# Kernel optimization log

Measured on AMD Instinct MI355X. Metric: run time of the kernel, lower is better.

The kernel has to match this reference:

```python
import jax, jax.numpy as jnp
import numpy as np

N, D, H, C, E, M = 8192, 256, 256, 64, 262144, 2048
WD = 5e-4   # weight_decay
HP1 = 0.9
TAU = 0.5


def _l2norm(x, eps=1e-12):
    n = jnp.sqrt(jnp.sum(x * x, axis=1, keepdims=True))
    return x / jnp.maximum(n, eps)


def setup_inputs() -> dict:
    key = jax.random.key(0)
    ks = jax.random.split(key, 20)
    s = 0.05
    return dict(
        features=jax.random.uniform(ks[0], (N, D), dtype=jnp.float32),
        support=jax.random.uniform(ks[1], (N, N), dtype=jnp.float32) / N,  # mimics normalized adjacency scale
        labels=jax.random.uniform(ks[2], (N, C), dtype=jnp.float32),
        mat01_intra=jax.random.uniform(ks[3], (M, M), dtype=jnp.float32),
        mat01_inter=jax.random.uniform(ks[4], (M, M), dtype=jnp.float32),
        W0=jax.random.normal(ks[5], (D, H), dtype=jnp.float32) * s,
        b0=jnp.zeros((H,), jnp.float32),
        W1=jax.random.normal(ks[6], (H, C), dtype=jnp.float32) * s,
        b1=jnp.zeros((C,), jnp.float32),
        Wh0=jax.random.normal(ks[7], (D, H), dtype=jnp.float32) * s,
        bh0=jnp.zeros((H,), jnp.float32),
        Wh1=jax.random.normal(ks[8], (H, C), dtype=jnp.float32) * s,
        bh1=jnp.zeros((C,), jnp.float32),
        Wc=jax.random.normal(ks[9], (2 * C, 1), dtype=jnp.float32) * s,
        bc=jnp.zeros((1,), jnp.float32),
        edge_pos_i=jax.random.randint(ks[10], (E,), 0, N, dtype=jnp.int32),
        edge_pos_j=jax.random.randint(ks[11], (E,), 0, N, dtype=jnp.int32),
        train_idx=jax.random.randint(ks[12], (M,), 0, N, dtype=jnp.int32),
        mask=jax.random.randint(ks[13], (N,), 0, 2, dtype=jnp.int32),
    )


def _forward(features, support, labels, mat01_intra, mat01_inter,
             W0, b0, W1, b1, Wh0, bh0, Wh1, bh1, Wc, bc,
             edge_pos_i, edge_pos_j, train_idx, mask):
    # --- GCN branch: relu(S (X W0) + b0) -> S (h0 W1) + b1
    h0 = jax.nn.relu(support @ (features @ W0) + b0)
    h1 = support @ (h0 @ W1) + b1
    gcn_n = _l2norm(h1)
    # --- HGCN branch (2-layer GCN stand-in)
    g0 = jax.nn.relu(support @ (features @ Wh0) + bh0)
    hgcn = support @ (g0 @ Wh1) + bh1
    hgcn_n = _l2norm(hgcn)
    outputs = _l2norm(0.6 * gcn_n + 0.4 * hgcn_n)

    # masked softmax cross entropy
    maskf = mask.astype(jnp.float32)
    maskf = maskf / jnp.mean(maskf)
    logp = jax.nn.log_softmax(outputs, axis=1)
    loss_ce = jnp.mean(-jnp.sum(labels * logp, axis=1) * maskf)

    # edge gathers + contra MLP: log sigmoid of linear on concatenated pairs
    yi_g, yj_g = gcn_n[edge_pos_i], gcn_n[edge_pos_j]
    yi_h, yj_h = hgcn_n[edge_pos_i], hgcn_n[edge_pos_j]
    z1 = jnp.concatenate([yi_g, yj_h], axis=1) @ Wc + bc  # [E,1]
    z2 = jnp.concatenate([yi_h, yj_g], axis=1) @ Wc + bc
    p_e_xy = -jnp.mean(jax.nn.log_sigmoid(z1)) - jnp.mean(jax.nn.log_sigmoid(z2))

    # unsupervised contrastive over full NxN
    cd1 = jnp.exp((gcn_n @ hgcn_n.T) / TAU)      # [N,N]
    pn1 = jnp.diagonal(cd1) / jnp.mean(cd1, axis=1)
    cd2 = jnp.exp((hgcn_n @ gcn_n.T) / TAU)
    pn2 = jnp.diagonal(cd2) / jnp.mean(cd2, axis=1)
    contra = -HP1 * jnp.mean(jnp.log(jnp.concatenate([pn1, pn2], axis=0)))

    # supervised contrastive on train subset
    rowsum = jnp.sum(mat01_intra, axis=1)  # mat01_intra_rowsum buffer
    h1t, h2t = gcn_n[train_idx], hgcn_n[train_idx]
    Mn = train_idx.shape[0]

    def sup(a, b):
        hc = jnp.exp((a @ b.T) / TAU)            # [M,M]
        sp = jnp.sum(hc * mat01_intra, axis=1)
        sn = (jnp.sum(hc * mat01_inter, axis=1) + sp) / (Mn - 1)
        return (sp / rowsum) / sn

    pns = jnp.concatenate([sup(h1t, h2t), sup(h2t, h1t)], axis=0)
    contra = contra + (-HP1 * jnp.mean(jnp.log(pns)))

    wd = WD * 0.5 * (jnp.sum(W0 ** 2) + jnp.sum(b0 ** 2) + jnp.sum(W1 ** 2)
                     + jnp.sum(b1 ** 2) + jnp.sum(Wc ** 2) + jnp.sum(bc ** 2))
    loss = loss_ce + 0.4 * p_e_xy + contra + wd  # HGCN.loss = 0 for the stand-in

    correct = (jnp.argmax(outputs, axis=1) == jnp.argmax(labels, axis=1)).astype(jnp.float32)
    accuracy = jnp.mean(correct * maskf)
    return outputs, loss, accuracy


def reference(features, support, labels, mat01_intra, mat01_inter,
              W0, b0, W1, b1, Wh0, bh0, Wh1, bh1, Wc, bc,
              edge_pos_i, edge_pos_j, train_idx, mask):
    return _forward(features, support, labels, mat01_intra, mat01_inter,
                    W0, b0, W1, b1, Wh0, bh0, Wh1, bh1, Wc, bc,
                    edge_pos_i, edge_pos_j, train_idx, mask)
```

## Files before the change

kernel.cpp:

```cpp
#include <hip/hip_runtime.h>

#define DEVI __device__ __forceinline__

typedef __bf16 bf16x8 __attribute__((ext_vector_type(8)));
typedef float f32x4 __attribute__((ext_vector_type(4)));
typedef unsigned short u16;
typedef unsigned long long ull;

constexpr int NN = 8192;
constexpr int EE = 262144;

constexpr size_t OF_WT0b = 0;
constexpr size_t OF_WT1b = OF_WT0b + 65536;
constexpr size_t OF_BIA0 = OF_WT1b + 32768;
constexpr size_t OF_X16  = OF_BIA0 + 512;
constexpr size_t OF_A    = OF_X16 + 1048576;
constexpr size_t OF_D    = OF_A + 2097152;
constexpr size_t OF_VEC  = OF_D + 524288;
constexpr size_t OF_SD   = OF_VEC;
constexpr size_t OF_R1   = OF_SD + 8192;
constexpr size_t OF_R2   = OF_R1 + 16384;
constexpr size_t OF_AG   = OF_R2 + 16384;
constexpr size_t OF_BG   = OF_AG + 8192;
constexpr size_t OF_AH   = OF_BG + 8192;
constexpr size_t OF_BH   = OF_AH + 8192;
constexpr size_t OF_SP1  = OF_BH + 8192;
constexpr size_t OF_SNR1 = OF_SP1 + 2048;
constexpr size_t OF_SP2  = OF_SNR1 + 2048;
constexpr size_t OF_SNR2 = OF_SP2 + 2048;
constexpr size_t OF_RSI  = OF_SNR2 + 2048;
constexpr size_t OF_SCAL = OF_RSI + 2048;
constexpr size_t WS_SMALL = OF_SCAL + 16;
constexpr size_t OF_S16  = WS_SMALL;
constexpr size_t OF_E    = OF_S16 + 33554432;
constexpr size_t WS_NEED = OF_E + 8388608;

#define SC_CE 0
#define SC_MASK 1
#define SC_ACC 2
#define SC_E1 3
#define SC_E2 4
#define SC_C1 5
#define SC_C2 6
#define SC_WD 7

DEVI u16 bf1(float f) { __bf16 h = (__bf16)f; return __builtin_bit_cast(u16, h); }
DEVI unsigned int bf2(float a, float b) {
  return (unsigned)bf1(a) | ((unsigned)bf1(b) << 16);
}
DEVI ull bf4(float4 v) {
  return (ull)bf2(v.x, v.y) | ((ull)bf2(v.z, v.w) << 32);
}
DEVI float b2f(u16 h) { return __uint_as_float(((unsigned)h) << 16); }
DEVI float lo16(unsigned w) { return __uint_as_float(w << 16); }
DEVI float hi16(unsigned w) { return __uint_as_float(w & 0xffff0000u); }
DEVI f32x4 mfma16(bf16x8 a, bf16x8 b, f32x4 c) {
  return __builtin_amdgcn_mfma_f32_16x16x32_bf16(a, b, c, 0, 0, 0);
}
DEVI float wsum64(float v) {
  #pragma unroll
  for (int m = 1; m < 64; m <<= 1) v += __shfl_xor(v, m, 64);
  return v;
}
DEVI float wmax64(float v) {
  #pragma unroll
  for (int m = 1; m < 64; m <<= 1) v = fmaxf(v, __shfl_xor(v, m, 64));
  return v;
}
DEVI int wargmax64(float v, int idx) {
  #pragma unroll
  for (int m = 1; m < 64; m <<= 1) {
    float ov = __shfl_xor(v, m, 64);
    int   oi = __shfl_xor(idx, m, 64);
    if (ov > v || (ov == v && oi < idx)) { v = ov; idx = oi; }
  }
  return idx;
}
DEVI void blockAtomicAdd(float* dst, float v) {
  __shared__ float red[4];
  const int tid = threadIdx.x;
  v = wsum64(v);
  __syncthreads();
  if ((tid & 63) == 0) red[tid >> 6] = v;
  __syncthreads();
  if (tid == 0) atomicAdd(dst, red[0] + red[1] + red[2] + red[3]);
}
DEVI float logsig(float z) {
  return fminf(z, 0.f) - log1pf(__expf(-fabsf(z)));
}

__global__ __launch_bounds__(256)
void cvtbf(const float* __restrict__ src, u16* __restrict__ dst, long n8) {
  long stride = (long)gridDim.x * 256;
  for (long i = (long)blockIdx.x * 256 + threadIdx.x; i < n8; i += stride) {
    long off = i << 3;
    float4 a = *(const float4*)(src + off);
    float4 b = *(const float4*)(src + off + 4);
    uint4 o;
    o.x = bf2(a.x, a.y); o.y = bf2(a.z, a.w);
    o.z = bf2(b.x, b.y); o.w = bf2(b.z, b.w);
    *(uint4*)(dst + off) = o;
  }
}

__global__ void prep(const float* __restrict__ W0, const float* __restrict__ Wh0,
                     const float* __restrict__ W1, const float* __restrict__ Wh1,
                     const float* __restrict__ b0, const float* __restrict__ bh0,
                     u16* __restrict__ wt0, u16* __restrict__ wt1,
                     float* __restrict__ bias0) {
  int t = blockIdx.x * 256 + threadIdx.x;
  if (t < 131072) {
    int j = t >> 8, k = t & 255;
    wt0[t] = bf1((j < 256) ? W0[k * 256 + j] : Wh0[k * 256 + (j - 256)]);
  } else if (t < 196608) {
    int u = t - 131072;
    int j = u >> 9, k = u & 511;
    float v = 0.f;
    if (j < 64)  { if (k < 256)  v = W1 [k * 64 + j]; }
    else         { if (k >= 256) v = Wh1[(k - 256) * 64 + (j - 64)]; }
    wt1[u] = bf1(v);
  } else if (t < 197120) {
    int j = t - 196608;
    bias0[j] = (j < 256) ? b0[j] : bh0[j - 256];
  }
}

template <int FM, int FN, int SWZ, int MLOC, int NLOG, int MINB>
__global__ __launch_bounds__(256, MINB)
void gemm_a(const u16* __restrict__ A16, const u16* __restrict__ B16,
            u16* __restrict__ Cv, int K, int Ntot, int ksteps, size_t splitStride) {
  constexpr int BM = 32 * FM, BN = 32 * FN;
  constexpr int NSEG = (BM + BN) / 16;
  constexpr int SPW = NSEG / 4;
  __shared__ __align__(16) u16 As[2][BM * 32];
  __shared__ __align__(16) u16 Bs[2][BN * 32];
  const int tid = threadIdx.x;
  const int l = tid & 63, wid = tid >> 6;
  const int wr = wid >> 1, wc = wid & 1;
  const int fr = l & 15, fg = l >> 4;

  int m0, n0;
  if (SWZ) {
    int id = blockIdx.x + gridDim.x * blockIdx.y;
    int e = id & 7, s = id >> 3;
    m0 = (e * MLOC + (s >> NLOG)) * BM;
    n0 = (s & ((1 << NLOG) - 1)) * BN;
  } else {
    m0 = blockIdx.y * BM;
    n0 = blockIdx.x * BN;
  }
  const size_t kbase = (size_t)blockIdx.z * ksteps * 32;

  const u16* gsrc[SPW];
  u16* ld0[SPW];
  u16* ld1[SPW];
  #pragma unroll
  for (int q = 0; q < SPW; ++q) {
    int s = q * 4 + wid;
    if (s < BM / 16) {
      gsrc[q] = A16 + (size_t)(m0 + s * 16 + (l & 15)) * K + kbase + ((l >> 4) << 3);
      ld0[q] = &As[0][s << 9];
      ld1[q] = &As[1][s << 9];
    } else {
      int t2 = s - BM / 16;
      gsrc[q] = B16 + (size_t)(n0 + t2 * 16 + (l & 15)) * K + kbase + ((l >> 4) << 3);
      ld0[q] = &Bs[0][t2 << 9];
      ld1[q] = &Bs[1][t2 << 9];
    }
  }
  auto stageTo = [&](int buf, int ks2) {
    int koff = ks2 * 32;
    #pragma unroll
    for (int q = 0; q < SPW; ++q) {
      u16* d = buf ? ld1[q] : ld0[q];
      __builtin_amdgcn_global_load_lds(
          (const __attribute__((address_space(1))) void*)(gsrc[q] + koff),
          (__attribute__((address_space(3))) void*)d, 16, 0, 0);
    }
  };

  f32x4 zero = {0.f, 0.f, 0.f, 0.f};
  f32x4 acc[FM][FN];
  #pragma unroll
  for (int i = 0; i < FM; ++i)
    #pragma unroll
    for (int j = 0; j < FN; ++j) acc[i][j] = zero;

  stageTo(0, 0);
  int cur = 0;
  for (int ks = 0; ks < ksteps; ++ks) {
    __syncthreads();
    if (ks + 1 < ksteps) stageTo(cur ^ 1, ks + 1);
    bf16x8 af[FM], bfv[FN];
    #pragma unroll
    for (int i = 0; i < FM; ++i)
      af[i] = *(const bf16x8*)&As[cur][((wr * FM + i) << 9) + (l << 3)];
    #pragma unroll
    for (int j = 0; j < FN; ++j)
      bfv[j] = *(const bf16x8*)&Bs[cur][((wc * FN + j) << 9) + (l << 3)];
    #pragma unroll
    for (int i = 0; i < FM; ++i)
      #pragma unroll
      for (int j = 0; j < FN; ++j)
        acc[i][j] = mfma16(af[i], bfv[j], acc[i][j]);
    cur ^= 1;
  }

  u16* outp = Cv + (size_t)blockIdx.z * splitStride;
  #pragma unroll
  for (int i = 0; i < FM; ++i)
    #pragma unroll
    for (int j = 0; j < FN; ++j)
      #pragma unroll
      for (int r = 0; r < 4; ++r) {
        int grow = m0 + wr * 16 * FM + i * 16 + (fg << 2) + r;
        int gcol = n0 + wc * 16 * FN + j * 16 + fr;
        outp[(size_t)grow * Ntot + gcol] = bf1(acc[i][j][r]);
      }
}

template <int NS>
__global__ __launch_bounds__(256)
void relupack(const u16* __restrict__ z, const float* __restrict__ bias,
              u16* __restrict__ h16) {
  int t = blockIdx.x * 256 + threadIdx.x;
  int off = t << 3;
  int col = off & 511;
  float4 c0 = *(const float4*)(bias + col);
  float4 c1 = *(const float4*)(bias + col + 4);
  float r[8] = {c0.x, c0.y, c0.z, c0.w, c1.x, c1.y, c1.z, c1.w};
  #pragma unroll
  for (int s = 0; s < NS; ++s) {
    uint4 a = *(const uint4*)(z + (size_t)s * 8192 * 512 + off);
    r[0] += lo16(a.x); r[1] += hi16(a.x);
    r[2] += lo16(a.y); r[3] += hi16(a.y);
    r[4] += lo16(a.z); r[5] += hi16(a.z);
    r[6] += lo16(a.w); r[7] += hi16(a.w);
  }
  uint4 o;
  o.x = bf2(fmaxf(r[0], 0.f), fmaxf(r[1], 0.f));
  o.y = bf2(fmaxf(r[2], 0.f), fmaxf(r[3], 0.f));
  o.z = bf2(fmaxf(r[4], 0.f), fmaxf(r[5], 0.f));
  o.w = bf2(fmaxf(r[6], 0.f), fmaxf(r[7], 0.f));
  *(uint4*)(h16 + off) = o;
}

template <int NS>
__global__ __launch_bounds__(256)
void rowstats(const u16* __restrict__ Z2p, const float* __restrict__ b1,
              const float* __restrict__ bh1, const float* __restrict__ labels,
              const int* __restrict__ mask, const float* __restrict__ Wc,
              float* __restrict__ outp, u16* __restrict__ gcn16, u16* __restrict__ hgcn16,
              float* __restrict__ sd, float* __restrict__ ag, float* __restrict__ bg,
              float* __restrict__ ah, float* __restrict__ bh, float* __restrict__ scal) {
  const int tid = threadIdx.x, l = tid & 63, w = tid >> 6;
  const float wa = Wc[l], wb = Wc[64 + l];
  const float bb1 = b1[l], bbh1 = bh1[l];
  float s_ce = 0.f, s_mk = 0.f, s_ac = 0.f;
  for (int it = 0; it < 8; ++it) {
    int row = blockIdx.x * 32 + it * 4 + w;
    float h1 = bb1, hg = bbh1;
    #pragma unroll
    for (int s = 0; s < NS; ++s) {
      h1 += b2f(Z2p[(size_t)s * 1048576 + row * 128 + l]);
      hg += b2f(Z2p[(size_t)s * 1048576 + row * 128 + 64 + l]);
    }
    float n1 = wsum64(h1 * h1);
    float gn = h1 / fmaxf(sqrtf(n1), 1e-12f);
    float n2 = wsum64(hg * hg);
    float hn = hg / fmaxf(sqrtf(n2), 1e-12f);
    float oc = 0.6f * gn + 0.4f * hn;
    float n3 = wsum64(oc * oc);
    float o = oc / fmaxf(sqrtf(n3), 1e-12f);
    size_t ro = (size_t)row * 64 + l;
    outp[ro] = o; gcn16[ro] = bf1(gn); hgcn16[ro] = bf1(hn);
    float sdv = wsum64(gn * hn);
    float vag = wsum64(gn * wa), vbg = wsum64(gn * wb);
    float vah = wsum64(hn * wa), vbh = wsum64(hn * wb);
    float lab = labels[ro];
    float mx = wmax64(o);
    float se = wsum64(__expf(o - mx));
    float lse = mx + __logf(se);
    float slab = wsum64(lab);
    float slo = wsum64(lab * o);
    int am_o = wargmax64(o, l);
    int am_l = wargmax64(lab, l);
    if (l == 0) {
      sd[row] = sdv; ag[row] = vag; bg[row] = vbg; ah[row] = vah; bh[row] = vbh;
      float mk = (float)mask[row];
      s_ce += (lse * slab - slo) * mk;
      s_mk += mk;
      s_ac += (am_o == am_l) ? mk : 0.f;
    }
  }
  blockAtomicAdd(&scal[SC_CE], s_ce);
  blockAtomicAdd(&scal[SC_MASK], s_mk);
  blockAtomicAdd(&scal[SC_ACC], s_ac);
}

__global__ __launch_bounds__(256)
void rowsumexp2(const u16* __restrict__ G16, const u16* __restrict__ H16,
                float* __restrict__ R1, float* __restrict__ R2) {
  constexpr int PK = 72;
  __shared__ __align__(16) u16 At[64 * PK];
  __shared__ __align__(16) u16 Bt[64 * PK];
  const int bx = blockIdx.x;
  const int nh = bx >> 8, r = bx & 255, dir = r >> 7;
  const u16* __restrict__ A = dir ? H16 : G16;
  const u16* __restrict__ B = dir ? G16 : H16;
  float* __restrict__ out = (dir ? R2 : R1) + nh * 8192;
  const int tid = threadIdx.x, l = tid & 63, w = tid >> 6;
  const int m0 = (r & 127) * 64;
  #pragma unroll
  for (int p = 0; p < 2; ++p) {
    int idx = p * 256 + tid, row = idx >> 3, kq = (idx & 7) << 3;
    *(uint4*)&At[row * PK + kq] = *(const uint4*)(A + (size_t)(m0 + row) * 64 + kq);
  }
  __syncthreads();
  const int fr = l & 15, fg = l >> 4;
  bf16x8 a0 = *(const bf16x8*)&At[(w * 16 + fr) * PK + (fg << 3)];
  bf16x8 a1 = *(const bf16x8*)&At[(w * 16 + fr) * PK + 32 + (fg << 3)];
  float rs0 = 0.f, rs1 = 0.f, rs2 = 0.f, rs3 = 0.f;
  const int nbeg = nh * 4096;
  for (int n0 = nbeg; n0 < nbeg + 4096; n0 += 64) {
    __syncthreads();
    #pragma unroll
    for (int p = 0; p < 2; ++p) {
      int idx = p * 256 + tid, row = idx >> 3, kq = (idx & 7) << 3;
      *(uint4*)&Bt[row * PK + kq] = *(const uint4*)(B + (size_t)(n0 + row) * 64 + kq);
    }
    __syncthreads();
    #pragma unroll
    for (int jn = 0; jn < 4; ++jn) {
      bf16x8 b0 = *(const bf16x8*)&Bt[(jn * 16 + fr) * PK + (fg << 3)];
      bf16x8 b1 = *(const bf16x8*)&Bt[(jn * 16 + fr) * PK + 32 + (fg << 3)];
      f32x4 c = {0.f, 0.f, 0.f, 0.f};
      c = mfma16(a0, b0, c);
      c = mfma16(a1, b1, c);
      rs0 += __expf(c[0] * 2.0f);
      rs1 += __expf(c[1] * 2.0f);
      rs2 += __expf(c[2] * 2.0f);
      rs3 += __expf(c[3] * 2.0f);
    }
  }
  #pragma unroll
  for (int m = 1; m < 16; m <<= 1) {
    rs0 += __shfl_xor(rs0, m, 64);
    rs1 += __shfl_xor(rs1, m, 64);
    rs2 += __shfl_xor(rs2, m, 64);
    rs3 += __shfl_xor(rs3, m, 64);
  }
  if (fr == 0) {
    int rb = m0 + w * 16 + fg * 4;
    out[rb + 0] = rs0; out[rb + 1] = rs1; out[rb + 2] = rs2; out[rb + 3] = rs3;
  }
}

__global__ __launch_bounds__(256)
void supstats2(const u16* __restrict__ G16, const u16* __restrict__ H16,
               const int* __restrict__ tidx,
               const float* __restrict__ Wi_g, const float* __restrict__ We_g,
               float* __restrict__ SP1, float* __restrict__ SNR1,
               float* __restrict__ SP2, float* __restrict__ SNR2) {
  constexpr int PK = 72;
  __shared__ __align__(16) u16 At[64 * PK];
  __shared__ __align__(16) u16 Bt[64 * PK];
  __shared__ float Ws0[64 * 68];
  __shared__ float Ws1[64 * 68];
  const int bx = blockIdx.x;
  const int chunk = bx >> 6, sub = bx & 63, dir = sub >> 5;
  const u16* __restrict__ A = dir ? H16 : G16;
  const u16* __restrict__ B = dir ? G16 : H16;
  float* __restrict__ sp_out  = dir ? SP2 : SP1;
  float* __restrict__ sn_out  = dir ? SNR2 : SNR1;
  const int tid = threadIdx.x, l = tid & 63, w = tid >> 6;
  const int m0 = (sub & 31) * 64;
  #pragma unroll
  for (int p = 0; p < 2; ++p) {
    int idx = p * 256 + tid, row = idx >> 3, kq = (idx & 7) << 3;
    int gr = tidx[m0 + row];
    *(uint4*)&At[row * PK + kq] = *(const uint4*)(A + (size_t)gr * 64 + kq);
  }
  __syncthreads();
  const int fr = l & 15, fg = l >> 4;
  bf16x8 a0 = *(const bf16x8*)&At[(w * 16 + fr) * PK + (fg << 3)];
  bf16x8 a1 = *(const bf16x8*)&At[(w * 16 + fr) * PK + 32 + (fg << 3)];
  float sp0 = 0, sp1 = 0, sp2 = 0, sp3 = 0, sn0 = 0, sn1 = 0, sn2 = 0, sn3 = 0;
  const int nbeg = chunk * 512;
  for (int n0 = nbeg; n0 < nbeg + 512; n0 += 64) {
    __syncthreads();
    #pragma unroll
    for (int p = 0; p < 2; ++p) {
      int idx = p * 256 + tid, row = idx >> 3, kq = (idx & 7) << 3;
      int gr = tidx[n0 + row];
      *(uint4*)&Bt[row * PK + kq] = *(const uint4*)(B + (size_t)gr * 64 + kq);
    }
    #pragma unroll
    for (int p = 0; p < 4; ++p) {
      int idx = p * 256 + tid, row = idx >> 4, kq = (idx & 15) << 2;
      *(float4*)&Ws0[row * 68 + kq] = *(const float4*)(Wi_g + (size_t)(m0 + row) * 2048 + n0 + kq);
      *(float4*)&Ws1[row * 68 + kq] = *(const float4*)(We_g + (size_t)(m0 + row) * 2048 + n0 + kq);
    }
    __syncthreads();
    #pragma unroll
    for (int jn = 0; jn < 4; ++jn) {
      bf16x8 b0 = *(const bf16x8*)&Bt[(jn * 16 + fr) * PK + (fg << 3)];
      bf16x8 b1 = *(const bf16x8*)&Bt[(jn * 16 + fr) * PK + 32 + (fg << 3)];
      f32x4 c = {0.f, 0.f, 0.f, 0.f};
      c = mfma16(a0, b0, c);
      c = mfma16(a1, b1, c);
      int cl = jn * 16 + fr;
      int rl = w * 16 + fg * 4;
      float e0 = __expf(c[0] * 2.0f);
      float e1 = __expf(c[1] * 2.0f);
      float e2 = __expf(c[2] * 2.0f);
      float e3 = __expf(c[3] * 2.0f);
      sp0 += e0 * Ws0[(rl + 0) * 68 + cl]; sn0 += e0 * Ws1[(rl + 0) * 68 + cl];
      sp1 += e1 * Ws0[(rl + 1) * 68 + cl]; sn1 += e1 * Ws1[(rl + 1) * 68 + cl];
      sp2 += e2 * Ws0[(rl + 2) * 68 + cl]; sn2 += e2 * Ws1[(rl + 2) * 68 + cl];
      sp3 += e3 * Ws0[(rl + 3) * 68 + cl]; sn3 += e3 * Ws1[(rl + 3) * 68 + cl];
    }
  }
  #pragma unroll
  for (int m = 1; m < 16; m <<= 1) {
    sp0 += __shfl_xor(sp0, m, 64); sn0 += __shfl_xor(sn0, m, 64);
    sp1 += __shfl_xor(sp1, m, 64); sn1 += __shfl_xor(sn1, m, 64);
    sp2 += __shfl_xor(sp2, m, 64); sn2 += __shfl_xor(sn2, m, 64);
    sp3 += __shfl_xor(sp3, m, 64); sn3 += __shfl_xor(sn3, m, 64);
  }
  if (fr == 0) {
    int rb = m0 + w * 16 + fg * 4;
    atomicAdd(&sp_out[rb + 0], sp0); atomicAdd(&sn_out[rb + 0], sn0);
    atomicAdd(&sp_out[rb + 1], sp1); atomicAdd(&sn_out[rb + 1], sn1);
    atomicAdd(&sp_out[rb + 2], sp2); atomicAdd(&sn_out[rb + 2], sn2);
    atomicAdd(&sp_out[rb + 3], sp3); atomicAdd(&sn_out[rb + 3], sn3);
  }
}

__global__ __launch_bounds__(256)
void rowsum2048(const float* __restrict__ Wi, float* __restrict__ rsi) {
  int l = threadIdx.x & 63, w = threadIdx.x >> 6;
  int row = blockIdx.x * 4 + w;
  float s = 0.f;
  #pragma unroll
  for (int p = 0; p < 8; ++p) {
    int c = (p * 64 + l) << 2;
    float4 v = *(const float4*)(Wi + (size_t)row * 2048 + c);
    s += v.x + v.y + v.z + v.w;
  }
  s = wsum64(s);
  if (l == 0) rsi[row] = s;
}

__global__ __launch_bounds__(256)
void edgered(const int* __restrict__ ei, const int* __restrict__ ej,
             const float* __restrict__ ag, const float* __restrict__ bg,
             const float* __restrict__ ah, const float* __restrict__ bh,
             const float* __restrict__ bc, float* __restrict__ scal) {
  int t = blockIdx.x * 256 + threadIdx.x;
  float bcv = bc[0];
  float s1 = 0.f, s2 = 0.f;
  for (int e = t; e < EE; e += 65536) {
    int i = ei[e], j = ej[e];
    s1 += logsig(ag[i] + bh[j] + bcv);
    s2 += logsig(ah[i] + bg[j] + bcv);
  }
  blockAtomicAdd(&scal[SC_E1], s1);
  blockAtomicAdd(&scal[SC_E2], s2);
}

__global__ __launch_bounds__(256)
void contrared(const float* __restrict__ sd, const float* __restrict__ r1,
               const float* __restrict__ r2, float* __restrict__ scal) {
  int i = blockIdx.x * 256 + threadIdx.x;
  constexpr float LOGN = 9.01091334728f;
  float ra = r1[i] + r1[8192 + i];
  float rb = r2[i] + r2[8192 + i];
  float v = 4.f * sd[i] - __logf(ra) - __logf(rb) + 2.f * LOGN;
  blockAtomicAdd(&scal[SC_C1], v);
}

__global__ __launch_bounds__(256)
void supred(const float* __restrict__ sp1, const float* __restrict__ snr1,
            const float* __restrict__ sp2, const float* __restrict__ snr2,
            const float* __restrict__ rsi, float* __restrict__ scal) {
  int i = blockIdx.x * 256 + threadIdx.x;
  float rs = rsi[i];
  float a1 = sp1[i], d1 = (snr1[i] + a1) * (1.f / 2047.f);
  float a2 = sp2[i], d2 = (snr2[i] + a2) * (1.f / 2047.f);
  float v = __logf(a1 / rs / d1) + __logf(a2 / rs / d2);
  blockAtomicAdd(&scal[SC_C2], v);
}

__global__ __launch_bounds__(256)
void wdsum(const float* __restrict__ W0, const float* __restrict__ b0,
           const float* __restrict__ W1, const float* __restrict__ b1,
           const float* __restrict__ Wc, const float* __restrict__ bc,
           float* __restrict__ scal) {
  int t = threadIdx.x;
  float s = 0.f;
  for (int i = t; i < 16384; i += 256) {
    float4 v = *(const float4*)(W0 + i * 4);
    s += v.x * v.x + v.y * v.y + v.z * v.z + v.w * v.w;
  }
  for (int i = t; i < 4096; i += 256) {
    float4 v = *(const float4*)(W1 + i * 4);
    s += v.x * v.x + v.y * v.y + v.z * v.z + v.w * v.w;
  }
  if (t < 256) { float v = b0[t]; s += v * v; }
  if (t < 64)  { float v = b1[t]; s += v * v; }
  if (t < 128) { float v = Wc[t]; s += v * v; }
  if (t == 0)  { float v = bc[0]; s += v * v; }
  blockAtomicAdd(&scal[SC_WD], s);
}

__global__ void finalk(const float* __restrict__ scal, float* __restrict__ dst) {
  float masks = scal[SC_MASK];
  float loss = scal[SC_CE] / masks
             + 0.4f * (-(scal[SC_E1] + scal[SC_E2]) * (1.f / 262144.f))
             - 0.9f * scal[SC_C1] * (1.f / 16384.f)
             - 0.9f * scal[SC_C2] * (1.f / 4096.f)
             + 5e-4f * 0.5f * scal[SC_WD];
  dst[0] = loss;
  dst[1] = scal[SC_ACC] / masks;
}

extern "C" void kernel_launch(void* const* d_in, const int* in_sizes, int n_in,
                              void* d_out, int out_size, void* d_ws, size_t ws_size,
                              hipStream_t stream) {
  const float* features = (const float*)d_in[0];
  const float* support  = (const float*)d_in[1];
  const float* labels   = (const float*)d_in[2];
  const float* intra    = (const float*)d_in[3];
  const float* inter    = (const float*)d_in[4];
  const float* W0  = (const float*)d_in[5];
  const float* b0  = (const float*)d_in[6];
  const float* W1  = (const float*)d_in[7];
  const float* b1  = (const float*)d_in[8];
  const float* Wh0 = (const float*)d_in[9];
  const float* bh0 = (const float*)d_in[10];
  const float* Wh1 = (const float*)d_in[11];
  const float* bh1 = (const float*)d_in[12];
  const float* Wc  = (const float*)d_in[13];
  const float* bc  = (const float*)d_in[14];
  const int* ei    = (const int*)d_in[15];
  const int* ej    = (const int*)d_in[16];
  const int* tidx  = (const int*)d_in[17];
  const int* mask  = (const int*)d_in[18];

  if (ws_size < WS_NEED * sizeof(float)) return;

  float* ws = (float*)d_ws;
  u16*   WT0b  = (u16*)(ws + OF_WT0b);
  u16*   WT1b  = (u16*)(ws + OF_WT1b);
  float* BIA0  = ws + OF_BIA0;
  u16*   X16   = (u16*)(ws + OF_X16);
  u16*   XWT16 = (u16*)(ws + OF_A);
  u16*   H16   = (u16*)(ws + OF_A);
  u16*   HWT16 = (u16*)(ws + OF_D);
  u16*   G16   = (u16*)(ws + OF_A);
  u16*   HG16  = (u16*)(ws + OF_A + 262144);
  u16*   S16   = (u16*)(ws + OF_S16);
  u16*   ZbS4  = (u16*)(ws + OF_E);
  u16*   Z2p16 = (u16*)(ws + OF_E);
  float* SD   = ws + OF_SD;
  float* R1   = ws + OF_R1;
  float* R2   = ws + OF_R2;
  float* AG   = ws + OF_AG;
  float* BG   = ws + OF_BG;
  float* AH   = ws + OF_AH;
  float* BH   = ws + OF_BH;
  float* SP1  = ws + OF_SP1;
  float* SNR1 = ws + OF_SNR1;
  float* SP2  = ws + OF_SP2;
  float* SNR2 = ws + OF_SNR2;
  float* RSI  = ws + OF_RSI;
  float* SCAL = ws + OF_SCAL;
  float* outp = (float*)d_out;

  hipMemsetAsync(SCAL, 0, 16 * sizeof(float), stream);
  hipMemsetAsync(SP1, 0, 4 * 2048 * sizeof(float), stream);
  prep<<<770, 256, 0, stream>>>(W0, Wh0, W1, Wh1, b0, bh0, WT0b, WT1b, BIA0);
  cvtbf<<<256, 256, 0, stream>>>(features, X16, 262144);
  cvtbf<<<4096, 256, 0, stream>>>(support, S16, 8388608);

  gemm_a<4, 4, 0, 0, 0, 4><<<dim3(64, 4, 1), 256, 0, stream>>>(
      WT0b, X16, XWT16, 256, 8192, 8, 0);

  gemm_a<8, 4, 1, 4, 2, 2><<<dim3(4, 32, 4), 256, 0, stream>>>(
      S16, XWT16, ZbS4, 8192, 512, 64, (size_t)8192 * 512);
  relupack<4><<<2048, 256, 0, stream>>>(ZbS4, BIA0, H16);

  gemm_a<2, 4, 0, 0, 0, 4><<<dim3(64, 2, 1), 256, 0, stream>>>(
      WT1b, H16, HWT16, 512, 8192, 16, 0);

  gemm_a<8, 4, 1, 4, 0, 2><<<dim3(1, 32, 16), 256, 0, stream>>>(
      S16, HWT16, Z2p16, 8192, 128, 16, (size_t)8192 * 128);
  rowstats<16><<<256, 256, 0, stream>>>(Z2p16, b1, bh1, labels, mask, Wc,
                                        outp, G16, HG16, SD, AG, BG, AH, BH, SCAL);

  rowsumexp2<<<512, 256, 0, stream>>>(G16, HG16, R1, R2);
  rowsum2048<<<512, 256, 0, stream>>>(intra, RSI);
  supstats2<<<256, 256, 0, stream>>>(G16, HG16, tidx, intra, inter,
                                     SP1, SNR1, SP2, SNR2);
  edgered<<<256, 256, 0, stream>>>(ei, ej, AG, BG, AH, BH, bc, SCAL);
  contrared<<<32, 256, 0, stream>>>(SD, R1, R2, SCAL);
  supred<<<8, 256, 0, stream>>>(SP1, SNR1, SP2, SNR2, RSI, SCAL);
  wdsum<<<1, 256, 0, stream>>>(W0, b0, W1, b1, Wc, bc, SCAL);
  finalk<<<1, 1, 0, stream>>>(SCAL, outp + (size_t)8192 * 64);
}
```

Measured before the change: 429.4 us.

## Compute both exp-similarity row and column sums from one G·Hᵀ pass

The rowsumexp kernel used to run two separate directions, G·Hᵀ and H·Gᵀ, each computing exp row sums. It now computes only G·Hᵀ and derives the second direction's sums as column sums. Column partials are reduced with shuffles, accumulated into a shared-memory buffer with atomics, and flushed to global R2 with atomics, which needs an extra memset of R2. This halves the MFMA and exp work but adds shared and global atomic traffic, a 16KB shared buffer that may lower occupancy, and a grid half the size.

New measurement: 475.8 us. 10.8% more time.

```diff
diff --git a/kernel.cpp b/kernel.cpp
--- a/kernel.cpp
+++ b/kernel.cpp
@@ -299,23 +299,23 @@
 }
 
 __global__ __launch_bounds__(256)
-void rowsumexp2(const u16* __restrict__ G16, const u16* __restrict__ H16,
+void rowsumexpc(const u16* __restrict__ G16, const u16* __restrict__ H16,
                 float* __restrict__ R1, float* __restrict__ R2) {
   constexpr int PK = 72;
   __shared__ __align__(16) u16 At[64 * PK];
   __shared__ __align__(16) u16 Bt[64 * PK];
+  __shared__ float colacc[4096];
   const int bx = blockIdx.x;
-  const int nh = bx >> 8, r = bx & 255, dir = r >> 7;
-  const u16* __restrict__ A = dir ? H16 : G16;
-  const u16* __restrict__ B = dir ? G16 : H16;
-  float* __restrict__ out = (dir ? R2 : R1) + nh * 8192;
+  const int nh = bx >> 7, mblk = bx & 127;
+  float* __restrict__ out1 = R1 + nh * 8192;
   const int tid = threadIdx.x, l = tid & 63, w = tid >> 6;
-  const int m0 = (r & 127) * 64;
+  const int m0 = mblk * 64;
   #pragma unroll
   for (int p = 0; p < 2; ++p) {
     int idx = p * 256 + tid, row = idx >> 3, kq = (idx & 7) << 3;
-    *(uint4*)&At[row * PK + kq] = *(const uint4*)(A + (size_t)(m0 + row) * 64 + kq);
-  }
+    *(uint4*)&At[row * PK + kq] = *(const uint4*)(G16 + (size_t)(m0 + row) * 64 + kq);
+  }
+  for (int i = tid; i < 4096; i += 256) colacc[i] = 0.f;
   __syncthreads();
   const int fr = l & 15, fg = l >> 4;
   bf16x8 a0 = *(const bf16x8*)&At[(w * 16 + fr) * PK + (fg << 3)];
@@ -327,7 +327,7 @@
     #pragma unroll
     for (int p = 0; p < 2; ++p) {
       int idx = p * 256 + tid, row = idx >> 3, kq = (idx & 7) << 3;
-      *(uint4*)&Bt[row * PK + kq] = *(const uint4*)(B + (size_t)(n0 + row) * 64 + kq);
+      *(uint4*)&Bt[row * PK + kq] = *(const uint4*)(H16 + (size_t)(n0 + row) * 64 + kq);
     }
     __syncthreads();
     #pragma unroll
@@ -337,10 +337,16 @@
       f32x4 c = {0.f, 0.f, 0.f, 0.f};
       c = mfma16(a0, b0, c);
       c = mfma16(a1, b1, c);
-      rs0 += __expf(c[0] * 2.0f);
-      rs1 += __expf(c[1] * 2.0f);
-      rs2 += __expf(c[2] * 2.0f);
-      rs3 += __expf(c[3] * 2.0f);
+      float e0 = __expf(c[0] * 2.0f);
+      float e1 = __expf(c[1] * 2.0f);
+      float e2 = __expf(c[2] * 2.0f);
+      float e3 = __expf(c[3] * 2.0f);
+      rs0 += e0; rs1 += e1; rs2 += e2; rs3 += e3;
+      float cv = (e0 + e1) + (e2 + e3);
+      cv += __shfl_xor(cv, 16, 64);
+      cv += __shfl_xor(cv, 32, 64);
+      if ((l & 48) == 0)
+        atomicAdd(&colacc[(n0 - nbeg) + jn * 16 + fr], cv);
     }
   }
   #pragma unroll
@@ -352,8 +358,11 @@
   }
   if (fr == 0) {
     int rb = m0 + w * 16 + fg * 4;
-    out[rb + 0] = rs0; out[rb + 1] = rs1; out[rb + 2] = rs2; out[rb + 3] = rs3;
-  }
+    out1[rb + 0] = rs0; out1[rb + 1] = rs1; out1[rb + 2] = rs2; out1[rb + 3] = rs3;
+  }
+  __syncthreads();
+  for (int i = tid; i < 4096; i += 256)
+    atomicAdd(&R2[nbeg + i], colacc[i]);
 }
 
 __global__ __launch_bounds__(256)
@@ -475,7 +484,7 @@
   int i = blockIdx.x * 256 + threadIdx.x;
   constexpr float LOGN = 9.01091334728f;
   float ra = r1[i] + r1[8192 + i];
-  float rb = r2[i] + r2[8192 + i];
+  float rb = r2[i];
   float v = 4.f * sd[i] - __logf(ra) - __logf(rb) + 2.f * LOGN;
   blockAtomicAdd(&scal[SC_C1], v);
 }
@@ -580,6 +589,7 @@
 
   hipMemsetAsync(SCAL, 0, 16 * sizeof(float), stream);
   hipMemsetAsync(SP1, 0, 4 * 2048 * sizeof(float), stream);
+  hipMemsetAsync(R2, 0, 8192 * sizeof(float), stream);
   prep<<<770, 256, 0, stream>>>(W0, Wh0, W1, Wh1, b0, bh0, WT0b, WT1b, BIA0);
   cvtbf<<<256, 256, 0, stream>>>(features, X16, 262144);
   cvtbf<<<4096, 256, 0, stream>>>(support, S16, 8388608);
@@ -599,7 +609,7 @@
   rowstats<16><<<256, 256, 0, stream>>>(Z2p16, b1, bh1, labels, mask, Wc,
                                         outp, G16, HG16, SD, AG, BG, AH, BH, SCAL);
 
-  rowsumexp2<<<512, 256, 0, stream>>>(G16, HG16, R1, R2);
+  rowsumexpc<<<256, 256, 0, stream>>>(G16, HG16, R1, R2);
   rowsum2048<<<512, 256, 0, stream>>>(intra, RSI);
   supstats2<<<256, 256, 0, stream>>>(G16, HG16, tidx, intra, inter,
                                      SP1, SNR1, SP2, SNR2);
```

## Add triple-buffered direct-to-LDS GEMM for the two support matmuls

Applied to the files above, without the earlier changes.

Adds a new GEMM kernel, gemm_c, and uses it for the two large support-matrix products. It stages tiles into a three-deep LDS ring using global_load_lds, waits only on the oldest loads with explicit vmcnt counts, and uses one barrier per k-step. LDS fragment reads are done with inline ds_read_b128 followed by a scheduling barrier. The goal is to overlap global memory traffic with MFMA work and cut synchronisation stalls. In exchange it uses more LDS per block and relies on ksteps leaving a remainder of 1 when divided by 3, which holds for the current call sites.

After: 439.7 us. 1.02x slower.

```diff
diff --git a/kernel.cpp b/kernel.cpp
--- a/kernel.cpp
+++ b/kernel.cpp
@@ -89,6 +89,20 @@
   return fminf(z, 0.f) - log1pf(__expf(-fabsf(z)));
 }
 
+template <int N> DEVI void vmwait() {
+  if constexpr (N == 0)      asm volatile("s_waitcnt vmcnt(0)" ::: "memory");
+  else if constexpr (N == 6) asm volatile("s_waitcnt vmcnt(6)" ::: "memory");
+  else                       asm volatile("s_waitcnt vmcnt(12)" ::: "memory");
+}
+DEVI bf16x8 dsr128(unsigned addr) {
+  bf16x8 r;
+  asm volatile("ds_read_b128 %0, %1" : "=v"(r) : "v"(addr));
+  return r;
+}
+DEVI unsigned ldsoff(const u16* p) {
+  return (unsigned)(size_t)(const __attribute__((address_space(3))) u16*)p;
+}
+
 __global__ __launch_bounds__(256)
 void cvtbf(const float* __restrict__ src, u16* __restrict__ dst, long n8) {
   long stride = (long)gridDim.x * 256;
@@ -204,6 +218,128 @@
       for (int j = 0; j < FN; ++j)
         acc[i][j] = mfma16(af[i], bfv[j], acc[i][j]);
     cur ^= 1;
+  }
+
+  u16* outp = Cv + (size_t)blockIdx.z * splitStride;
+  #pragma unroll
+  for (int i = 0; i < FM; ++i)
+    #pragma unroll
+    for (int j = 0; j < FN; ++j)
+      #pragma unroll
+      for (int r = 0; r < 4; ++r) {
+        int grow = m0 + wr * 16 * FM + i * 16 + (fg << 2) + r;
+        int gcol = n0 + wc * 16 * FN + j * 16 + fr;
+        outp[(size_t)grow * Ntot + gcol] = bf1(acc[i][j][r]);
+      }
+}
+
+template <int FM, int FN, int SWZ, int MLOC, int NLOG>
+__global__ __launch_bounds__(256, 2)
+void gemm_c(const u16* __restrict__ A16, const u16* __restrict__ B16,
+            u16* __restrict__ Cv, int K, int Ntot, int ksteps, size_t splitStride) {
+  constexpr int BM = 32 * FM, BN = 32 * FN;
+  constexpr int NSEG = (BM + BN) / 16;
+  constexpr int SPW = NSEG / 4;
+  constexpr int ASZ = BM * 32, BSZ = BN * 32;
+  constexpr unsigned ABY = ASZ * 2, BBY = BSZ * 2;
+  __shared__ __align__(16) u16 As[3][ASZ];
+  __shared__ __align__(16) u16 Bs[3][BSZ];
+  const int tid = threadIdx.x;
+  const int l = tid & 63, wid = tid >> 6;
+  const int wr = wid >> 1, wc = wid & 1;
+  const int fr = l & 15, fg = l >> 4;
+
+  int m0, n0;
+  if (SWZ) {
+    int id = blockIdx.x + gridDim.x * blockIdx.y;
+    int e = id & 7, s = id >> 3;
+    m0 = (e * MLOC + (s >> NLOG)) * BM;
+    n0 = (s & ((1 << NLOG) - 1)) * BN;
+  } else {
+    m0 = blockIdx.y * BM;
+    n0 = blockIdx.x * BN;
+  }
+  const size_t kbase = (size_t)blockIdx.z * ksteps * 32;
+
+  const u16* gsrc[SPW];
+  u16* ldb[SPW];
+  int  lstr[SPW];
+  #pragma unroll
+  for (int q = 0; q < SPW; ++q) {
+    int s = q * 4 + wid;
+    if (s < BM / 16) {
+      gsrc[q] = A16 + (size_t)(m0 + s * 16 + (l & 15)) * K + kbase + ((l >> 4) << 3);
+      ldb[q] = &As[0][s << 9];
+      lstr[q] = ASZ;
+    } else {
+      int t2 = s - BM / 16;
+      gsrc[q] = B16 + (size_t)(n0 + t2 * 16 + (l & 15)) * K + kbase + ((l >> 4) << 3);
+      ldb[q] = &Bs[0][t2 << 9];
+      lstr[q] = BSZ;
+    }
+  }
+  auto stageTo = [&](int buf, int ks2) {
+    int koff = ks2 * 32;
+    #pragma unroll
+    for (int q = 0; q < SPW; ++q) {
+      u16* d = ldb[q] + buf * lstr[q];
+      __builtin_amdgcn_global_load_lds(
+          (const __attribute__((address_space(1))) void*)(gsrc[q] + koff),
+          (__attribute__((address_space(3))) void*)d, 16, 0, 0);
+    }
+  };
+
+  const unsigned aBase = ldsoff(&As[0][0]) + ((unsigned)(wr * FM) << 10) + ((unsigned)l << 4);
+  const unsigned bBase = ldsoff(&Bs[0][0]) + ((unsigned)(wc * FN) << 10) + ((unsigned)l << 4);
+
+  f32x4 zero = {0.f, 0.f, 0.f, 0.f};
+  f32x4 acc[FM][FN];
+  #pragma unroll
+  for (int i = 0; i < FM; ++i)
+    #pragma unroll
+    for (int j = 0; j < FN; ++j) acc[i][j] = zero;
+
+  stageTo(0, 0);
+  stageTo(1, 1);
+
+  for (int ks = 0; ks + 1 < ksteps; ks += 3) {
+    #pragma unroll
+    for (int u = 0; u < 3; ++u) {
+      const int t = ks + u;
+      vmwait<SPW>();
+      __builtin_amdgcn_s_barrier();
+      if (t + 2 < ksteps) stageTo((u + 2) % 3, t + 2);
+      bf16x8 af[FM], bfv[FN];
+      const unsigned aab = aBase + (unsigned)u * ABY;
+      const unsigned bbb = bBase + (unsigned)u * BBY;
+      #pragma unroll
+      for (int i = 0; i < FM; ++i) af[i] = dsr128(aab + ((unsigned)i << 10));
+      #pragma unroll
+      for (int j = 0; j < FN; ++j) bfv[j] = dsr128(bbb + ((unsigned)j << 10));
+      asm volatile("s_waitcnt lgkmcnt(0)" ::: "memory");
+      __builtin_amdgcn_sched_barrier(0);
+      #pragma unroll
+      for (int i = 0; i < FM; ++i)
+        #pragma unroll
+        for (int j = 0; j < FN; ++j)
+          acc[i][j] = mfma16(af[i], bfv[j], acc[i][j]);
+    }
+  }
+  {
+    vmwait<0>();
+    __builtin_amdgcn_s_barrier();
+    bf16x8 af[FM], bfv[FN];
+    #pragma unroll
+    for (int i = 0; i < FM; ++i) af[i] = dsr128(aBase + ((unsigned)i << 10));
+    #pragma unroll
+    for (int j = 0; j < FN; ++j) bfv[j] = dsr128(bBase + ((unsigned)j << 10));
+    asm volatile("s_waitcnt lgkmcnt(0)" ::: "memory");
+    __builtin_amdgcn_sched_barrier(0);
+    #pragma unroll
+    for (int i = 0; i < FM; ++i)
+      #pragma unroll
+      for (int j = 0; j < FN; ++j)
+        acc[i][j] = mfma16(af[i], bfv[j], acc[i][j]);
   }
 
   u16* outp = Cv + (size_t)blockIdx.z * splitStride;
@@ -587,14 +723,14 @@
   gemm_a<4, 4, 0, 0, 0, 4><<<dim3(64, 4, 1), 256, 0, stream>>>(
       WT0b, X16, XWT16, 256, 8192, 8, 0);
 
-  gemm_a<8, 4, 1, 4, 2, 2><<<dim3(4, 32, 4), 256, 0, stream>>>(
+  gemm_c<8, 4, 1, 4, 2><<<dim3(4, 32, 4), 256, 0, stream>>>(
       S16, XWT16, ZbS4, 8192, 512, 64, (size_t)8192 * 512);
   relupack<4><<<2048, 256, 0, stream>>>(ZbS4, BIA0, H16);
 
   gemm_a<2, 4, 0, 0, 0, 4><<<dim3(64, 2, 1), 256, 0, stream>>>(
       WT1b, H16, HWT16, 512, 8192, 16, 0);
 
-  gemm_a<8, 4, 1, 4, 0, 2><<<dim3(1, 32, 16), 256, 0, stream>>>(
+  gemm_c<8, 4, 1, 4, 0><<<dim3(1, 32, 16), 256, 0, stream>>>(
       S16, HWT16, Z2p16, 8192, 128, 16, (size_t)8192 * 128);
   rowstats<16><<<256, 256, 0, stream>>>(Z2p16, b1, bh1, labels, mask, Wc,
                                         outp, G16, HG16, SD, AG, BG, AH, BH, SCAL);
```
